# Optimization experiments

Measured on AMD Instinct MI355X. Metric: run time of the kernel, lower is better.

Reference implementation:

```python
import jax, jax.numpy as jnp
import numpy as np

N_NODES = 50000


def _glorot(key, fan_in, fan_out):
    limit = float(np.sqrt(6.0 / (fan_in + fan_out)))
    return jax.random.uniform(key, (fan_in, fan_out), jnp.float32, -limit, limit)


def setup_inputs() -> dict:
    key = jax.random.key(0)
    k_x, k_src, k_dst, k1, k2, k3 = jax.random.split(key, 6)
    x = jax.random.normal(k_x, (N_NODES, 128), dtype=jnp.float32)
    src = jax.random.randint(k_src, (800000,), 0, N_NODES)
    dst = jax.random.randint(k_dst, (800000,), 0, N_NODES)
    edge_index = jnp.stack([src, dst]).astype(jnp.int64)  # [2, E]
    W1 = _glorot(k1, 128, 96)
    W2 = _glorot(k2, 96, 96)
    W3 = _glorot(k3, 96, 40)
    b1 = jnp.zeros((96,), jnp.float32)
    b2 = jnp.zeros((96,), jnp.float32)
    b3 = jnp.zeros((40,), jnp.float32)
    return {"x": x, "W1": W1, "b1": b1, "W2": W2, "b2": b2,
            "W3": W3, "b3": b3, "edge_index": edge_index}


def _aggregate(x, src, dst):
    # sparse adj SpMM with 'add' reduce: out[dst] += x[src]
    return jax.ops.segment_sum(x[src], dst, num_segments=N_NODES)


def reference(x, W1, b1, W2, b2, W3, b3, edge_index):
    src, dst = edge_index[0], edge_index[1]
    # layer 1: aggregate -> linear -> relu (dropout identity in eval)
    h = jax.nn.relu(_aggregate(x, src, dst) @ W1 + b1)
    # layer 2
    h = jax.nn.relu(_aggregate(h, src, dst) @ W2 + b2)
    # layer 3 + log_softmax
    logits = _aggregate(h, src, dst) @ W3 + b3
    return jax.nn.log_softmax(logits, axis=-1)
```

## Files before the change

### kernel.cpp

```cpp
#include <hip/hip_runtime.h>
#include <math.h>

typedef __attribute__((ext_vector_type(8))) short bf16x8;
typedef __attribute__((ext_vector_type(4))) float f32x4;

__device__ __forceinline__ unsigned short f2bf(float f) {
  unsigned u = __float_as_uint(f);
  u += 0x7fffu + ((u >> 16) & 1u);
  return (unsigned short)(u >> 16);
}
__device__ __forceinline__ float bflo(unsigned u) { return __uint_as_float(u << 16); }
__device__ __forceinline__ float bfhi(unsigned u) { return __uint_as_float(u & 0xffff0000u); }

#define ACC8(U)                                           \
  a0 += bflo(U.x); a1 += bfhi(U.x); a2 += bflo(U.y); a3 += bfhi(U.y); \
  a4 += bflo(U.z); a5 += bfhi(U.z); a6 += bflo(U.w); a7 += bfhi(U.w)


constexpr int EB = 4096;
constexpr int QT = 64;
constexpr int SLOT = 3072;

__device__ __forceinline__ void gemm1_tile(int bx, int tid, const float* __restrict__ x,
                                           const uint4* __restrict__ sW,
                                           unsigned short* __restrict__ Tb, int N) {
  int wid = tid >> 6;
  int lane = tid & 63;
  int rt = bx * 4 + wid;
  if (rt * 16 >= N) return;
  int quad = lane >> 4;
  int lm = lane & 15;
  union BU { uint4 u; bf16x8 v; };
  f32x4 acc[6];
#pragma unroll
  for (int c = 0; c < 6; ++c) acc[c] = (f32x4){0.f, 0.f, 0.f, 0.f};
  int row = rt * 16 + lm;
  if (row >= N) row = N - 1;
#pragma unroll
  for (int s = 0; s < 4; ++s) {
    int k0 = s * 32 + quad * 8;
    const float* Af = x + (size_t)row * 128 + k0;
    float4 x0 = *(const float4*)(Af);
    float4 x1 = *(const float4*)(Af + 4);
    union { unsigned short s[8]; bf16x8 v; } au;
    au.s[0] = f2bf(x0.x); au.s[1] = f2bf(x0.y); au.s[2] = f2bf(x0.z); au.s[3] = f2bf(x0.w);
    au.s[4] = f2bf(x1.x); au.s[5] = f2bf(x1.y); au.s[6] = f2bf(x1.z); au.s[7] = f2bf(x1.w);
#pragma unroll
    for (int c = 0; c < 6; ++c) {
      BU bu;
      bu.u = sW[(s * 6 + c) * 64 + lane];
      acc[c] = __builtin_amdgcn_mfma_f32_16x16x32_bf16(au.v, bu.v, acc[c], 0, 0, 0);
    }
  }
#pragma unroll
  for (int c = 0; c < 6; ++c) {
    int colv = c * 16 + lm;
#pragma unroll
    for (int r = 0; r < 4; ++r) {
      int orow = rt * 16 + quad * 4 + r;
      if (orow < N) Tb[(size_t)orow * 96 + colv] = f2bf(acc[c][r]);
    }
  }
}

struct BinSM {
  int lcnt[512];
  int lstart[512];
  int cur[512];
  int stage[EB];
};
union D1SM {
  BinSM b;
  uint4 sW[1536];
};

__global__ __launch_bounds__(256) void d1_bin_gemm_pack(
    const int* __restrict__ src, const int* __restrict__ dst,
    int* __restrict__ partial, int* __restrict__ packed,
    const float* __restrict__ x, const float* __restrict__ W1,
    const float* __restrict__ W2, const float* __restrict__ W3,
    unsigned short* __restrict__ Wp2, unsigned short* __restrict__ Wp3,
    unsigned short* __restrict__ Tb, int E, int N, int NBv, int NBIN, int GB) {
  __shared__ D1SM sm;
  int tid = threadIdx.x;
  if ((int)blockIdx.x < NBIN) {
    int* lcnt = sm.b.lcnt;
    int* lstart = sm.b.lstart;
    int* cur = sm.b.cur;
    int* stage = sm.b.stage;
    lcnt[tid] = 0;
    lcnt[tid + 256] = 0;
    __syncthreads();
    int E4 = E >> 2;
    int base4 = blockIdx.x * (EB >> 2);
    int sv[16], dv[16];
    int nv = 0;
#pragma unroll
    for (int j = 0; j < 4; ++j) {
      int idx4 = base4 + j * 256 + tid;
      if (idx4 < E4 && idx4 < base4 + (EB >> 2)) {
        int4 s4 = ((const int4*)src)[idx4];
        int4 d4 = ((const int4*)dst)[idx4];
        sv[j * 4 + 0] = s4.x; dv[j * 4 + 0] = d4.x;
        sv[j * 4 + 1] = s4.y; dv[j * 4 + 1] = d4.y;
        sv[j * 4 + 2] = s4.z; dv[j * 4 + 2] = d4.z;
        sv[j * 4 + 3] = s4.w; dv[j * 4 + 3] = d4.w;
        nv = j * 4 + 4;
      }
    }
#pragma unroll
    for (int i = 0; i < 16; ++i)
      if (i < nv) atomicAdd(&lcnt[dv[i] >> 7], 1);
    bool last = ((int)blockIdx.x == NBIN - 1);
    int tl = E & 3;
    if (last && tid == 0)
      for (int t = 0; t < tl; ++t) atomicAdd(&lcnt[dst[E4 * 4 + t] >> 7], 1);
    __syncthreads();
    lstart[tid] = lcnt[tid];
    lstart[tid + 256] = lcnt[tid + 256];
    __syncthreads();
    for (int off = 1; off < 512; off <<= 1) {
      int a0 = (tid >= off) ? lstart[tid - off] : 0;
      int i1 = tid + 256;
      int a1 = (i1 >= off) ? lstart[i1 - off] : 0;
      __syncthreads();
      lstart[tid] += a0;
      lstart[i1] += a1;
      __syncthreads();
    }
    int e0 = lstart[tid] - lcnt[tid];
    int e1 = lstart[tid + 256] - lcnt[tid + 256];
    __syncthreads();
    lstart[tid] = e0; cur[tid] = e0;
    lstart[tid + 256] = e1; cur[tid + 256] = e1;
    __syncthreads();
#pragma unroll
    for (int i = 0; i < 16; ++i)
      if (i < nv) {
        int b = dv[i] >> 7;
        int p = atomicAdd(&cur[b], 1);
        stage[p] = ((dv[i] & 127) << 16) | (sv[i] & 0xffff);
      }
    if (last && tid == 0)
      for (int t = 0; t < tl; ++t) {
        int d = dst[E4 * 4 + t], s = src[E4 * 4 + t];
        int p = atomicAdd(&cur[d >> 7], 1);
        stage[p] = ((d & 127) << 16) | (s & 0xffff);
      }
    int c0 = lcnt[tid]; if (c0 > QT) c0 = QT;
    int c1 = lcnt[tid + 256]; if (c1 > QT) c1 = QT;
    partial[blockIdx.x * 512 + tid] = c0;
    partial[blockIdx.x * 512 + tid + 256] = c1;
    __syncthreads();
    int meB = lstart[511] + lcnt[511];
    for (int i = tid; i < meB; i += 256) {
      int lo = 0, hi = 511;
      while (lo < hi) {
        int mid = (lo + hi + 1) >> 1;
        if (lstart[mid] <= i) lo = mid; else hi = mid - 1;
      }
      int j = i - lstart[lo];
      if (j < QT) packed[((size_t)blockIdx.x * NBv + lo) * QT + j] = stage[i];
    }
    return;
  }
  int gb = blockIdx.x - NBIN;
  if (gb < GB) {
#pragma unroll
    for (int k = 0; k < 6; ++k) {
      int t = tid + k * 256;
      int lane = t & 63;
      int frag = t >> 6;
      int s = frag / 6;
      int ct = frag - s * 6;
      int colv = ct * 16 + (lane & 15);
      int k0 = s * 32 + (lane >> 4) * 8;
      union { unsigned short h[8]; uint4 u; } pk;
#pragma unroll
      for (int j = 0; j < 8; ++j) pk.h[j] = f2bf(W1[(k0 + j) * 96 + colv]);
      sm.sW[t] = pk.u;
    }
    __syncthreads();
    gemm1_tile(gb, tid, x, sm.sW, Tb, N);
    return;
  }
  int gid = (gb - GB) * 256 + tid;
  const float* W;
  unsigned short* Wp;
  int t, NCTT, M, MV;
  if (gid < 1152) {
    W = W2; Wp = Wp2; t = gid; NCTT = 6; M = 96; MV = 96;
  } else if (gid < 1728) {
    W = W3; Wp = Wp3; t = gid - 1152; NCTT = 3; M = 40; MV = 40;
  } else {
    return;
  }
  int lane = t & 63;
  int frag = t >> 6;
  int s = frag / NCTT;
  int ct = frag - s * NCTT;
  int colv = ct * 16 + (lane & 15);
  int k0 = s * 32 + (lane >> 4) * 8;
  union { unsigned short h[8]; uint4 u; } pk;
#pragma unroll
  for (int j = 0; j < 8; ++j) {
    float v = (colv < MV) ? W[(k0 + j) * M + colv] : 0.f;
    pk.h[j] = f2bf(v);
  }
  ((uint4*)Wp)[t] = pk.u;
}

__global__ __launch_bounds__(256) void build_csr(const int* __restrict__ partial,
                                                 const int* __restrict__ packed,
                                                 int* __restrict__ row_ptr,
                                                 int* __restrict__ degA,
                                                 int* __restrict__ col, int N, int NBv,
                                                 int NBIN) {
  __shared__ int e[257];
  __shared__ int stage[SLOT];
  __shared__ int cnt[512];
  __shared__ int scn[512];
  __shared__ int cur[512];
  int tid = threadIdx.x;
  int b = blockIdx.x;
  int c = (tid < NBIN) ? partial[tid * 512 + b] : 0;
  e[tid] = c;
  __syncthreads();
  for (int off = 1; off < 256; off <<= 1) {
    int a = (tid >= off) ? e[tid - off] : 0;
    __syncthreads();
    e[tid] += a;
    __syncthreads();
  }
  int excl = e[tid] - c;
  __syncthreads();
  e[tid] = excl;
  if (tid == 255) e[256] = excl + c;
  __syncthreads();
  int me = e[256];
  if (me > SLOT) me = SLOT;
  for (int i = tid; i < me; i += 256) {
    int lo = 0, hi = 255;
    while (lo < hi) {
      int mid = (lo + hi + 1) >> 1;
      if (e[mid] <= i) lo = mid; else hi = mid - 1;
    }
    stage[i] = packed[((size_t)lo * NBv + b) * QT + (i - e[lo])];
  }
  cnt[tid] = 0;
  cnt[tid + 256] = 0;
  __syncthreads();
  for (int i = tid; i < me; i += 256) {
    int pk = stage[i];
    int bin = ((pk >> 16) << 2) | ((pk >> 14) & 3);
    atomicAdd(&cnt[bin], 1);
  }
  __syncthreads();
  scn[tid] = cnt[tid];
  scn[tid + 256] = cnt[tid + 256];
  __syncthreads();
  for (int off = 1; off < 512; off <<= 1) {
    int a0 = (tid >= off) ? scn[tid - off] : 0;
    int i1 = tid + 256;
    int a1 = (i1 >= off) ? scn[i1 - off] : 0;
    __syncthreads();
    scn[tid] += a0;
    scn[i1] += a1;
    __syncthreads();
  }
  int ex0 = scn[tid] - cnt[tid];
  int ex1 = scn[tid + 256] - cnt[tid + 256];
  cur[tid] = b * SLOT + ex0;
  cur[tid + 256] = b * SLOT + ex1;
  __syncthreads();
  int node0 = b << 7;
  int RL = N - node0;
  if (RL > 128) RL = 128;
  if (tid < RL) {
    int bb = tid << 2;
    int beg = scn[bb] - cnt[bb];
    row_ptr[node0 + tid] = b * SLOT + beg;
    degA[node0 + tid] = scn[bb + 3] - beg;
  }
  for (int i = tid; i < me; i += 256) {
    int pk = stage[i];
    int bin = ((pk >> 16) << 2) | ((pk >> 14) & 3);
    int p = atomicAdd(&cur[bin], 1);
    col[p] = pk & 0xffff;
  }
}


template <int NCT, int MOUT, int MVALID>
__global__ __launch_bounds__(256, 8) void fused_agg_gemm(
    const unsigned short* __restrict__ tin, const int* __restrict__ row_ptr,
    const int* __restrict__ degA, const int* __restrict__ col,
    const float* __restrict__ bias, const unsigned short* __restrict__ Wp,
    unsigned short* __restrict__ outp, int N) {
  constexpr int LST = 104;
  constexpr int CAP = 1536;
  __shared__ unsigned short sH[64 * LST];
  __shared__ int scol[CAP];
  __shared__ int srp[64];
  __shared__ int sdeg[64];
  __shared__ short sperm[64];
  int tid = threadIdx.x;
  int node0 = blockIdx.x * 64;
  int nloc = N - node0;
  if (nloc > 64) nloc = 64;
  if (tid < nloc) srp[tid] = row_ptr[node0 + tid];
  if (tid < 64) sdeg[tid] = (tid < nloc) ? degA[node0 + tid] : 0x7fffffff;
  __syncthreads();
  int gs = srp[0];
  int me = srp[nloc - 1] + sdeg[nloc - 1] - gs;
  for (int i = tid; i < me && i < CAP; i += 256) scol[i] = col[gs + i];
  if (tid < 64) {
    int ki = sdeg[tid];
    int rank = 0;
#pragma unroll 8
    for (int j = 0; j < 64; ++j) {
      int kj = sdeg[j];
      rank += (kj < ki) || (kj == ki && j < tid);
    }
    sperm[rank] = (short)tid;
  }
  __syncthreads();
  bool fits = (me <= CAP);

#pragma unroll
  for (int it = 0; it < 3; ++it) {
    int u = tid + it * 256;
    int sl = u / 12;
    int c = u - sl * 12;
    int nl = sperm[sl];
    if (nl < nloc) {
      int beg = srp[nl] - gs;
      int end = beg + sdeg[nl];
      const unsigned short* tc = tin + 8 * c;
      float a0 = 0.f, a1 = 0.f, a2 = 0.f, a3 = 0.f, a4 = 0.f, a5 = 0.f, a6 = 0.f, a7 = 0.f;
      if (fits) {
        int e = beg;
        for (; e + 3 < end; e += 4) {
          int s0 = scol[e], s1 = scol[e + 1], s2 = scol[e + 2], s3 = scol[e + 3];
          uint4 u0 = *(const uint4*)(tc + (size_t)s0 * 96);
          uint4 u1 = *(const uint4*)(tc + (size_t)s1 * 96);
          uint4 u2 = *(const uint4*)(tc + (size_t)s2 * 96);
          uint4 u3 = *(const uint4*)(tc + (size_t)s3 * 96);
          ACC8(u0); ACC8(u1); ACC8(u2); ACC8(u3);
        }
        for (; e < end; ++e) {
          int s0 = scol[e];
          uint4 u4 = *(const uint4*)(tc + (size_t)s0 * 96);
          ACC8(u4);
        }
      } else {
        for (int e = beg; e < end; ++e) {
          int s0 = col[gs + e];
          uint4 u4 = *(const uint4*)(tc + (size_t)s0 * 96);
          ACC8(u4);
        }
      }
      const float* b = bias + 8 * c;
      union { unsigned short s[8]; uint4 u; } pk;
      pk.s[0] = f2bf(fmaxf(a0 + b[0], 0.f));
      pk.s[1] = f2bf(fmaxf(a1 + b[1], 0.f));
      pk.s[2] = f2bf(fmaxf(a2 + b[2], 0.f));
      pk.s[3] = f2bf(fmaxf(a3 + b[3], 0.f));
      pk.s[4] = f2bf(fmaxf(a4 + b[4], 0.f));
      pk.s[5] = f2bf(fmaxf(a5 + b[5], 0.f));
      pk.s[6] = f2bf(fmaxf(a6 + b[6], 0.f));
      pk.s[7] = f2bf(fmaxf(a7 + b[7], 0.f));
      *(uint4*)&sH[sl * LST + c * 8] = pk.u;
    }
  }
  __syncthreads();

  int wid = tid >> 6;
  int lane = tid & 63;
  int rt16 = wid * 16;
  if (rt16 >= nloc) return;
  int quad = lane >> 4;
  int lm = lane & 15;
  union BU { uint4 u; bf16x8 v; };
  f32x4 acc[NCT];
#pragma unroll
  for (int c = 0; c < NCT; ++c) acc[c] = (f32x4){0.f, 0.f, 0.f, 0.f};
  const uint4* wp4 = (const uint4*)Wp;
#pragma unroll
  for (int s = 0; s < 3; ++s) {
    BU au;
    au.u = *(const uint4*)&sH[(rt16 + lm) * LST + s * 32 + quad * 8];
#pragma unroll
    for (int c = 0; c < NCT; ++c) {
      BU bu;
      bu.u = wp4[(s * NCT + c) * 64 + lane];
      acc[c] = __builtin_amdgcn_mfma_f32_16x16x32_bf16(au.v, bu.v, acc[c], 0, 0, 0);
    }
  }
#pragma unroll
  for (int c = 0; c < NCT; ++c) {
    int colv = c * 16 + lm;
    if (colv >= MVALID) continue;
#pragma unroll
    for (int r = 0; r < 4; ++r) {
      int nl_o = sperm[rt16 + quad * 4 + r];
      if (nl_o < nloc) outp[(size_t)(node0 + nl_o) * MOUT + colv] = f2bf(acc[c][r]);
    }
  }
}

__global__ __launch_bounds__(256) void agg_lsm_bf16(const unsigned short* __restrict__ t,
                                                    const int* __restrict__ row_ptr,
                                                    const int* __restrict__ degA,
                                                    const int* __restrict__ col,
                                                    const float* __restrict__ bias,
                                                    float* __restrict__ out, int N) {
  constexpr int CAPL = 1024;
  __shared__ int scol[CAPL];
  __shared__ int srp[16];
  __shared__ int sdeg[16];
  __shared__ short sperm[16];
  int tid = threadIdx.x;
  int node0 = blockIdx.x * 16;
  int nloc = N - node0;
  if (nloc > 16) nloc = 16;
  if (tid < nloc) srp[tid] = row_ptr[node0 + tid];
  if (tid < 16) sdeg[tid] = (tid < nloc) ? degA[node0 + tid] : 0x7fffffff;
  __syncthreads();
  int gs = srp[0];
  int me = srp[nloc - 1] + sdeg[nloc - 1] - gs;
  for (int i = tid; i < me && i < CAPL; i += 256) scol[i] = col[gs + i];
  if (tid < 16) {
    int ki = sdeg[tid];
    int rank = 0;
#pragma unroll
    for (int j = 0; j < 16; ++j) {
      int kj = sdeg[j];
      rank += (kj < ki) || (kj == ki && j < tid);
    }
    sperm[rank] = (short)tid;
  }
  __syncthreads();
  bool fits = (me <= CAPL);

  int sl = tid >> 4;
  int c = tid & 15;
  int nl = sperm[sl];
  bool act = (c < 10) && (nl < nloc);
  int ceff = (c < 10) ? c : 0;
  const unsigned short* tc = t + 4 * ceff;
  float v0 = 0.f, v1 = 0.f, v2 = 0.f, v3 = 0.f;
  if (act) {
    int beg = srp[nl] - gs;
    int end = beg + sdeg[nl];
    if (fits) {
      int e = beg;
      for (; e + 7 < end; e += 8) {
        uint2 g0 = *(const uint2*)(tc + (size_t)scol[e] * 64);
        uint2 g1 = *(const uint2*)(tc + (size_t)scol[e + 1] * 64);
        uint2 g2 = *(const uint2*)(tc + (size_t)scol[e + 2] * 64);
        uint2 g3 = *(const uint2*)(tc + (size_t)scol[e + 3] * 64);
        uint2 g4 = *(const uint2*)(tc + (size_t)scol[e + 4] * 64);
        uint2 g5 = *(const uint2*)(tc + (size_t)scol[e + 5] * 64);
        uint2 g6 = *(const uint2*)(tc + (size_t)scol[e + 6] * 64);
        uint2 g7 = *(const uint2*)(tc + (size_t)scol[e + 7] * 64);
        v0 += bflo(g0.x); v1 += bfhi(g0.x); v2 += bflo(g0.y); v3 += bfhi(g0.y);
        v0 += bflo(g1.x); v1 += bfhi(g1.x); v2 += bflo(g1.y); v3 += bfhi(g1.y);
        v0 += bflo(g2.x); v1 += bfhi(g2.x); v2 += bflo(g2.y); v3 += bfhi(g2.y);
        v0 += bflo(g3.x); v1 += bfhi(g3.x); v2 += bflo(g3.y); v3 += bfhi(g3.y);
        v0 += bflo(g4.x); v1 += bfhi(g4.x); v2 += bflo(g4.y); v3 += bfhi(g4.y);
        v0 += bflo(g5.x); v1 += bfhi(g5.x); v2 += bflo(g5.y); v3 += bfhi(g5.y);
        v0 += bflo(g6.x); v1 += bfhi(g6.x); v2 += bflo(g6.y); v3 += bfhi(g6.y);
        v0 += bflo(g7.x); v1 += bfhi(g7.x); v2 += bflo(g7.y); v3 += bfhi(g7.y);
      }
      for (; e + 3 < end; e += 4) {
        uint2 g0 = *(const uint2*)(tc + (size_t)scol[e] * 64);
        uint2 g1 = *(const uint2*)(tc + (size_t)scol[e + 1] * 64);
        uint2 g2 = *(const uint2*)(tc + (size_t)scol[e + 2] * 64);
        uint2 g3 = *(const uint2*)(tc + (size_t)scol[e + 3] * 64);
        v0 += bflo(g0.x); v1 += bfhi(g0.x); v2 += bflo(g0.y); v3 += bfhi(g0.y);
        v0 += bflo(g1.x); v1 += bfhi(g1.x); v2 += bflo(g1.y); v3 += bfhi(g1.y);
        v0 += bflo(g2.x); v1 += bfhi(g2.x); v2 += bflo(g2.y); v3 += bfhi(g2.y);
        v0 += bflo(g3.x); v1 += bfhi(g3.x); v2 += bflo(g3.y); v3 += bfhi(g3.y);
      }
      for (; e < end; ++e) {
        uint2 g0 = *(const uint2*)(tc + (size_t)scol[e] * 64);
        v0 += bflo(g0.x); v1 += bfhi(g0.x); v2 += bflo(g0.y); v3 += bfhi(g0.y);
      }
    } else {
      for (int e = beg; e < end; ++e) {
        uint2 g0 = *(const uint2*)(tc + (size_t)col[gs + e] * 64);
        v0 += bflo(g0.x); v1 += bfhi(g0.x); v2 += bflo(g0.y); v3 += bfhi(g0.y);
      }
    }
  }
  const float* bb = bias + 4 * ceff;
  v0 += bb[0]; v1 += bb[1]; v2 += bb[2]; v3 += bb[3];
  float m = act ? fmaxf(fmaxf(v0, v1), fmaxf(v2, v3)) : -__builtin_inff();
#pragma unroll
  for (int off = 8; off; off >>= 1) m = fmaxf(m, __shfl_xor(m, off, 64));
  float ex = act ? (__expf(v0 - m) + __expf(v1 - m) + __expf(v2 - m) + __expf(v3 - m)) : 0.f;
#pragma unroll
  for (int off = 8; off; off >>= 1) ex += __shfl_xor(ex, off, 64);
  if (act) {
    int node = node0 + nl;
    float l = m + __logf(ex);
    float* o = out + (size_t)node * 40 + 4 * c;
    o[0] = v0 - l; o[1] = v1 - l; o[2] = v2 - l; o[3] = v3 - l;
  }
}


extern "C" void kernel_launch(void* const* d_in, const int* in_sizes, int n_in,
                              void* d_out, int out_size, void* d_ws, size_t ws_size,
                              hipStream_t stream) {
  const float* x  = (const float*)d_in[0];
  const float* W1 = (const float*)d_in[1];
  const float* b1 = (const float*)d_in[2];
  const float* W2 = (const float*)d_in[3];
  const float* b2 = (const float*)d_in[4];
  const float* W3 = (const float*)d_in[5];
  const float* b3 = (const float*)d_in[6];
  const int* edge = (const int*)d_in[7];

  int N = in_sizes[0] / 128;
  int E = in_sizes[7] / 2;
  const int* srcp = edge;
  const int* dstp = edge + E;

  char* p = (char*)d_ws;
  auto alloc = [&](size_t bytes) {
    char* r = p;
    p += (bytes + 255) & ~size_t(255);
    return r;
  };
  int NB = (N + 127) >> 7;
  int NBIN = (E + EB - 1) / EB;
  int GB = ((N + 15) / 16 + 3) / 4;
  int PB = 7;
  int FB = (N + 63) / 64;

  int* partial = (int*)alloc((size_t)NBIN * 512 * 4);
  int* packed  = (int*)alloc((size_t)NBIN * NB * QT * 4);
  int* row_ptr = (int*)alloc((size_t)N * 4);
  int* degA    = (int*)alloc((size_t)N * 4);
  int* col     = (int*)alloc((size_t)NB * SLOT * 4);
  unsigned short* Wp2 = (unsigned short*)alloc(1152 * 8 * 2);
  unsigned short* Wp3 = (unsigned short*)alloc(576 * 8 * 2);
  unsigned short* Tb  = (unsigned short*)alloc((size_t)N * 96 * 2);
  unsigned short* T2b = (unsigned short*)alloc((size_t)N * 96 * 2);
  unsigned short* T3b = (unsigned short*)alloc((size_t)N * 64 * 2);

  d1_bin_gemm_pack<<<NBIN + GB + PB, 256, 0, stream>>>(srcp, dstp, partial, packed,
                                                       x, W1, W2, W3, Wp2, Wp3, Tb,
                                                       E, N, NB, NBIN, GB);
  build_csr<<<NB, 256, 0, stream>>>(partial, packed, row_ptr, degA, col, N, NB, NBIN);
  fused_agg_gemm<6, 96, 96><<<FB, 256, 0, stream>>>(Tb, row_ptr, degA, col, b1, Wp2, T2b, N);
  fused_agg_gemm<3, 64, 40><<<FB, 256, 0, stream>>>(T2b, row_ptr, degA, col, b2, Wp3, T3b, N);
  agg_lsm_bf16<<<(N + 15) / 16, 256, 0, stream>>>(T3b, row_ptr, degA, col, b3, (float*)d_out, N);
}
```

Baseline: 184.3 us.

## Split neighbor gathers into four source-range phases with block barriers

```diff
diff --git a/kernel.cpp b/kernel.cpp
--- a/kernel.cpp
+++ b/kernel.cpp
@@ -214,6 +214,7 @@
                                                  const int* __restrict__ packed,
                                                  int* __restrict__ row_ptr,
                                                  int* __restrict__ degA,
+                                                 int* __restrict__ rp4,
                                                  int* __restrict__ col, int N, int NBv,
                                                  int NBIN) {
   __shared__ int e[257];
@@ -282,6 +283,11 @@
     row_ptr[node0 + tid] = b * SLOT + beg;
     degA[node0 + tid] = scn[bb + 3] - beg;
   }
+  {
+    int n0 = tid >> 2, n1 = (tid + 256) >> 2;
+    if (n0 < RL) rp4[(size_t)(node0 + n0) * 4 + (tid & 3)] = b * SLOT + ex0;
+    if (n1 < RL) rp4[(size_t)(node0 + n1) * 4 + (tid & 3)] = b * SLOT + ex1;
+  }
   for (int i = tid; i < me; i += 256) {
     int pk = stage[i];
     int bin = ((pk >> 16) << 2) | ((pk >> 14) & 3);
@@ -294,15 +300,17 @@
 template <int NCT, int MOUT, int MVALID>
 __global__ __launch_bounds__(256, 8) void fused_agg_gemm(
     const unsigned short* __restrict__ tin, const int* __restrict__ row_ptr,
-    const int* __restrict__ degA, const int* __restrict__ col,
+    const int* __restrict__ degA, const int* __restrict__ rp4,
+    const int* __restrict__ col,
     const float* __restrict__ bias, const unsigned short* __restrict__ Wp,
     unsigned short* __restrict__ outp, int N) {
   constexpr int LST = 104;
-  constexpr int CAP = 1536;
+  constexpr int CAP = 1280;
   __shared__ unsigned short sH[64 * LST];
   __shared__ int scol[CAP];
   __shared__ int srp[64];
   __shared__ int sdeg[64];
+  __shared__ int s4rp[64][4];
   __shared__ short sperm[64];
   int tid = threadIdx.x;
   int node0 = blockIdx.x * 64;
@@ -310,6 +318,7 @@
   if (nloc > 64) nloc = 64;
   if (tid < nloc) srp[tid] = row_ptr[node0 + tid];
   if (tid < 64) sdeg[tid] = (tid < nloc) ? degA[node0 + tid] : 0x7fffffff;
+  if (tid < 4 * nloc) s4rp[tid >> 2][tid & 3] = rp4[(size_t)(node0 + (tid >> 2)) * 4 + (tid & 3)];
   __syncthreads();
   int gs = srp[0];
   int me = srp[nloc - 1] + sdeg[nloc - 1] - gs;
@@ -333,33 +342,42 @@
     int sl = u / 12;
     int c = u - sl * 12;
     int nl = sperm[sl];
-    if (nl < nloc) {
-      int beg = srp[nl] - gs;
-      int end = beg + sdeg[nl];
-      const unsigned short* tc = tin + 8 * c;
-      float a0 = 0.f, a1 = 0.f, a2 = 0.f, a3 = 0.f, a4 = 0.f, a5 = 0.f, a6 = 0.f, a7 = 0.f;
-      if (fits) {
-        int e = beg;
-        for (; e + 3 < end; e += 4) {
-          int s0 = scol[e], s1 = scol[e + 1], s2 = scol[e + 2], s3 = scol[e + 3];
-          uint4 u0 = *(const uint4*)(tc + (size_t)s0 * 96);
-          uint4 u1 = *(const uint4*)(tc + (size_t)s1 * 96);
-          uint4 u2 = *(const uint4*)(tc + (size_t)s2 * 96);
-          uint4 u3 = *(const uint4*)(tc + (size_t)s3 * 96);
-          ACC8(u0); ACC8(u1); ACC8(u2); ACC8(u3);
-        }
-        for (; e < end; ++e) {
-          int s0 = scol[e];
-          uint4 u4 = *(const uint4*)(tc + (size_t)s0 * 96);
-          ACC8(u4);
-        }
-      } else {
-        for (int e = beg; e < end; ++e) {
-          int s0 = col[gs + e];
-          uint4 u4 = *(const uint4*)(tc + (size_t)s0 * 96);
-          ACC8(u4);
+    bool valid = (nl < nloc);
+    const unsigned short* tc = tin + 8 * c;
+    float a0 = 0.f, a1 = 0.f, a2 = 0.f, a3 = 0.f, a4 = 0.f, a5 = 0.f, a6 = 0.f, a7 = 0.f;
+    int beg0 = valid ? (srp[nl] - gs) : 0;
+    int dtot = valid ? sdeg[nl] : 0;
+#pragma unroll
+    for (int t = 0; t < 4; ++t) {
+      if (valid) {
+        int bt = s4rp[nl][t] - gs;
+        int et = (t < 3) ? (s4rp[nl][t + 1] - gs) : (beg0 + dtot);
+        if (fits) {
+          int e = bt;
+          for (; e + 3 < et; e += 4) {
+            int s0 = scol[e], s1 = scol[e + 1], s2 = scol[e + 2], s3 = scol[e + 3];
+            uint4 u0 = *(const uint4*)(tc + (size_t)s0 * 96);
+            uint4 u1 = *(const uint4*)(tc + (size_t)s1 * 96);
+            uint4 u2 = *(const uint4*)(tc + (size_t)s2 * 96);
+            uint4 u3 = *(const uint4*)(tc + (size_t)s3 * 96);
+            ACC8(u0); ACC8(u1); ACC8(u2); ACC8(u3);
+          }
+          for (; e < et; ++e) {
+            int s0 = scol[e];
+            uint4 u4 = *(const uint4*)(tc + (size_t)s0 * 96);
+            ACC8(u4);
+          }
+        } else {
+          for (int e = bt; e < et; ++e) {
+            int s0 = col[gs + e];
+            uint4 u4 = *(const uint4*)(tc + (size_t)s0 * 96);
+            ACC8(u4);
+          }
         }
       }
+      __syncthreads();
+    }
+    if (valid) {
       const float* b = bias + 8 * c;
       union { unsigned short s[8]; uint4 u; } pk;
       pk.s[0] = f2bf(fmaxf(a0 + b[0], 0.f));
@@ -412,6 +430,7 @@
 __global__ __launch_bounds__(256) void agg_lsm_bf16(const unsigned short* __restrict__ t,
                                                     const int* __restrict__ row_ptr,
                                                     const int* __restrict__ degA,
+                                                    const int* __restrict__ rp4,
                                                     const int* __restrict__ col,
                                                     const float* __restrict__ bias,
                                                     float* __restrict__ out, int N) {
@@ -419,6 +438,7 @@
   __shared__ int scol[CAPL];
   __shared__ int srp[16];
   __shared__ int sdeg[16];
+  __shared__ int s4[16][4];
   __shared__ short sperm[16];
   int tid = threadIdx.x;
   int node0 = blockIdx.x * 16;
@@ -426,6 +446,7 @@
   if (nloc > 16) nloc = 16;
   if (tid < nloc) srp[tid] = row_ptr[node0 + tid];
   if (tid < 16) sdeg[tid] = (tid < nloc) ? degA[node0 + tid] : 0x7fffffff;
+  if (tid < 4 * nloc) s4[tid >> 2][tid & 3] = rp4[(size_t)(node0 + (tid >> 2)) * 4 + (tid & 3)];
   __syncthreads();
   int gs = srp[0];
   int me = srp[nloc - 1] + sdeg[nloc - 1] - gs;
@@ -450,49 +471,37 @@
   int ceff = (c < 10) ? c : 0;
   const unsigned short* tc = t + 4 * ceff;
   float v0 = 0.f, v1 = 0.f, v2 = 0.f, v3 = 0.f;
-  if (act) {
-    int beg = srp[nl] - gs;
-    int end = beg + sdeg[nl];
-    if (fits) {
-      int e = beg;
-      for (; e + 7 < end; e += 8) {
-        uint2 g0 = *(const uint2*)(tc + (size_t)scol[e] * 64);
-        uint2 g1 = *(const uint2*)(tc + (size_t)scol[e + 1] * 64);
-        uint2 g2 = *(const uint2*)(tc + (size_t)scol[e + 2] * 64);
-        uint2 g3 = *(const uint2*)(tc + (size_t)scol[e + 3] * 64);
-        uint2 g4 = *(const uint2*)(tc + (size_t)scol[e + 4] * 64);
-        uint2 g5 = *(const uint2*)(tc + (size_t)scol[e + 5] * 64);
-        uint2 g6 = *(const uint2*)(tc + (size_t)scol[e + 6] * 64);
-        uint2 g7 = *(const uint2*)(tc + (size_t)scol[e + 7] * 64);
-        v0 += bflo(g0.x); v1 += bfhi(g0.x); v2 += bflo(g0.y); v3 += bfhi(g0.y);
-        v0 += bflo(g1.x); v1 += bfhi(g1.x); v2 += bflo(g1.y); v3 += bfhi(g1.y);
-        v0 += bflo(g2.x); v1 += bfhi(g2.x); v2 += bflo(g2.y); v3 += bfhi(g2.y);
-        v0 += bflo(g3.x); v1 += bfhi(g3.x); v2 += bflo(g3.y); v3 += bfhi(g3.y);
-        v0 += bflo(g4.x); v1 += bfhi(g4.x); v2 += bflo(g4.y); v3 += bfhi(g4.y);
-        v0 += bflo(g5.x); v1 += bfhi(g5.x); v2 += bflo(g5.y); v3 += bfhi(g5.y);
-        v0 += bflo(g6.x); v1 += bfhi(g6.x); v2 += bflo(g6.y); v3 += bfhi(g6.y);
-        v0 += bflo(g7.x); v1 += bfhi(g7.x); v2 += bflo(g7.y); v3 += bfhi(g7.y);
+  int beg0 = act ? (srp[nl] - gs) : 0;
+  int dtot = act ? sdeg[nl] : 0;
+#pragma unroll
+  for (int tt = 0; tt < 4; ++tt) {
+    if (act) {
+      int bt = s4[nl][tt] - gs;
+      int et = (tt < 3) ? (s4[nl][tt + 1] - gs) : (beg0 + dtot);
+      if (fits) {
+        int e = bt;
+        for (; e + 3 < et; e += 4) {
+          uint2 g0 = *(const uint2*)(tc + (size_t)scol[e] * 64);
+          uint2 g1 = *(const uint2*)(tc + (size_t)scol[e + 1] * 64);
+          uint2 g2 = *(const uint2*)(tc + (size_t)scol[e + 2] * 64);
+          uint2 g3 = *(const uint2*)(tc + (size_t)scol[e + 3] * 64);
+          v0 += bflo(g0.x); v1 += bfhi(g0.x); v2 += bflo(g0.y); v3 += bfhi(g0.y);
+          v0 += bflo(g1.x); v1 += bfhi(g1.x); v2 += bflo(g1.y); v3 += bfhi(g1.y);
+          v0 += bflo(g2.x); v1 += bfhi(g2.x); v2 += bflo(g2.y); v3 += bfhi(g2.y);
+          v0 += bflo(g3.x); v1 += bfhi(g3.x); v2 += bflo(g3.y); v3 += bfhi(g3.y);
+        }
+        for (; e < et; ++e) {
+          uint2 g0 = *(const uint2*)(tc + (size_t)scol[e] * 64);
+          v0 += bflo(g0.x); v1 += bfhi(g0.x); v2 += bflo(g0.y); v3 += bfhi(g0.y);
+        }
+      } else {
+        for (int e = bt; e < et; ++e) {
+          uint2 g0 = *(const uint2*)(tc + (size_t)col[gs + e] * 64);
+          v0 += bflo(g0.x); v1 += bfhi(g0.x); v2 += bflo(g0.y); v3 += bfhi(g0.y);
+        }
       }
-      for (; e + 3 < end; e += 4) {
-        uint2 g0 = *(const uint2*)(tc + (size_t)scol[e] * 64);
-        uint2 g1 = *(const uint2*)(tc + (size_t)scol[e + 1] * 64);
-        uint2 g2 = *(const uint2*)(tc + (size_t)scol[e + 2] * 64);
-        uint2 g3 = *(const uint2*)(tc + (size_t)scol[e + 3] * 64);
-        v0 += bflo(g0.x); v1 += bfhi(g0.x); v2 += bflo(g0.y); v3 += bfhi(g0.y);
-        v0 += bflo(g1.x); v1 += bfhi(g1.x); v2 += bflo(g1.y); v3 += bfhi(g1.y);
-        v0 += bflo(g2.x); v1 += bfhi(g2.x); v2 += bflo(g2.y); v3 += bfhi(g2.y);
-        v0 += bflo(g3.x); v1 += bfhi(g3.x); v2 += bflo(g3.y); v3 += bfhi(g3.y);
-      }
-      for (; e < end; ++e) {
-        uint2 g0 = *(const uint2*)(tc + (size_t)scol[e] * 64);
-        v0 += bflo(g0.x); v1 += bfhi(g0.x); v2 += bflo(g0.y); v3 += bfhi(g0.y);
-      }
-    } else {
-      for (int e = beg; e < end; ++e) {
-        uint2 g0 = *(const uint2*)(tc + (size_t)col[gs + e] * 64);
-        v0 += bflo(g0.x); v1 += bfhi(g0.x); v2 += bflo(g0.y); v3 += bfhi(g0.y);
-      }
-    }
+    }
+    __syncthreads();
   }
   const float* bb = bias + 4 * ceff;
   v0 += bb[0]; v1 += bb[1]; v2 += bb[2]; v3 += bb[3];
@@ -544,6 +553,7 @@
   int* packed  = (int*)alloc((size_t)NBIN * NB * QT * 4);
   int* row_ptr = (int*)alloc((size_t)N * 4);
   int* degA    = (int*)alloc((size_t)N * 4);
+  int* rp4     = (int*)alloc((size_t)N * 4 * 4);
   int* col     = (int*)alloc((size_t)NB * SLOT * 4);
   unsigned short* Wp2 = (unsigned short*)alloc(1152 * 8 * 2);
   unsigned short* Wp3 = (unsigned short*)alloc(576 * 8 * 2);
@@ -554,8 +564,8 @@
   d1_bin_gemm_pack<<<NBIN + GB + PB, 256, 0, stream>>>(srcp, dstp, partial, packed,
                                                        x, W1, W2, W3, Wp2, Wp3, Tb,
                                                        E, N, NB, NBIN, GB);
-  build_csr<<<NB, 256, 0, stream>>>(partial, packed, row_ptr, degA, col, N, NB, NBIN);
-  fused_agg_gemm<6, 96, 96><<<FB, 256, 0, stream>>>(Tb, row_ptr, degA, col, b1, Wp2, T2b, N);
-  fused_agg_gemm<3, 64, 40><<<FB, 256, 0, stream>>>(T2b, row_ptr, degA, col, b2, Wp3, T3b, N);
-  agg_lsm_bf16<<<(N + 15) / 16, 256, 0, stream>>>(T3b, row_ptr, degA, col, b3, (float*)d_out, N);
-}
+  build_csr<<<NB, 256, 0, stream>>>(partial, packed, row_ptr, degA, rp4, col, N, NB, NBIN);
+  fused_agg_gemm<6, 96, 96><<<FB, 256, 0, stream>>>(Tb, row_ptr, degA, rp4, col, b1, Wp2, T2b, N);
+  fused_agg_gemm<3, 64, 40><<<FB, 256, 0, stream>>>(T2b, row_ptr, degA, rp4, col, b2, Wp3, T3b, N);
+  agg_lsm_bf16<<<(N + 15) / 16, 256, 0, stream>>>(T3b, row_ptr, degA, rp4, col, b3, (float*)d_out, N);
+}
```

Result: slower. 205.6 us (+11.5%).
